# Kernel tuning notes

Measured on AMD Instinct MI355X. Metric: run time of the kernel, lower is better.

The kernel has to match this reference:

```python
import jax, jax.numpy as jnp
import numpy as np

NUM_CLASSES = 100  # matches labels fill_max
N, D = 131072, 512


def setup_inputs() -> dict:
    key = jax.random.key(0)
    kf, kl = jax.random.split(key)
    features = jax.random.normal(kf, (N, D), dtype=jnp.float32)
    labels = jax.random.randint(kl, (N,), 0, NUM_CLASSES, dtype=jnp.int64)
    return {"features": features, "labels": labels}


def reference(features, labels):
    # Per-class segment reductions: counts, sum of features, sum of squared norms.
    # trace(cov_c) = (sum_i ||x_i||^2 - n_c * ||mu_c||^2) / (n_c - 1)
    ones = jnp.ones((features.shape[0],), dtype=features.dtype)
    counts = jax.ops.segment_sum(ones, labels, num_segments=NUM_CLASSES)          # [C]
    sums = jax.ops.segment_sum(features, labels, num_segments=NUM_CLASSES)        # [C, D]
    sq = jax.ops.segment_sum(jnp.sum(features * features, axis=1), labels,
                             num_segments=NUM_CLASSES)                            # [C]
    safe_n = jnp.maximum(counts, 1.0)
    mu = sums / safe_n[:, None]                                                   # [C, D]
    ssd = sq - counts * jnp.sum(mu * mu, axis=1)                                  # sum sq deviations
    trace = ssd / jnp.maximum(counts - 1.0, 1.0)                                  # [C]
    valid = counts >= 2.0
    valid_count = jnp.sum(valid.astype(features.dtype))
    total = jnp.sum(jnp.where(valid, trace, 0.0))
    loss = jnp.where(valid_count > 0, total / jnp.maximum(valid_count, 1.0), 0.0)
    return loss
```

## Files before the change

kernel.cpp:

```cpp
#include <hip/hip_runtime.h>

#define NCLASS 100
#define DDIM   512
#define NROWS  131072

#define CHUNK   1024
#define NCHUNK  (NROWS / CHUNK)
#define NSLICE  2
#define THREADS 1024
#define NWAVES  16

__global__ __launch_bounds__(THREADS) void icv_accum_kernel(
    const float* __restrict__ feat,
    const int*   __restrict__ labels,
    float*       __restrict__ sums_p,
    float*       __restrict__ sq_p,
    int*         __restrict__ cnt_p)
{
    __shared__ int s_cnt[NCLASS];
    __shared__ int s_off[NCLASS + 1];
    __shared__ int s_pos[NCLASS];
    __shared__ int s_scan[128];
    __shared__ int s_rows[CHUNK];

    const int tid   = threadIdx.x;
    const int wave  = tid >> 6;
    const int lane  = tid & 63;
    const int slice = blockIdx.x & (NSLICE - 1);
    const int chunk = blockIdx.x >> 1;
    const int row0  = chunk * CHUNK;

    if (tid < NCLASS) s_cnt[tid] = 0;
    __syncthreads();
    const int mylab = labels[row0 + tid];
    atomicAdd(&s_cnt[mylab], 1);
    __syncthreads();

    if (tid < 128) s_scan[tid] = (tid < NCLASS) ? s_cnt[tid] : 0;
    __syncthreads();
    #pragma unroll
    for (int d = 1; d < 128; d <<= 1) {
        int v = 0;
        if (tid < 128) { v = s_scan[tid]; if (tid >= d) v += s_scan[tid - d]; }
        __syncthreads();
        if (tid < 128) s_scan[tid] = v;
        __syncthreads();
    }
    if (tid < NCLASS) {
        const int e = s_scan[tid] - s_cnt[tid];
        s_off[tid] = e;
        s_pos[tid] = e;
    }
    if (tid == NCLASS) s_off[NCLASS] = CHUNK;
    __syncthreads();
    {
        const int p = atomicAdd(&s_pos[mylab], 1);
        s_rows[p] = tid;
    }
    if (slice == 0 && tid < NCLASS)
        cnt_p[chunk * NCLASS + tid] = s_cnt[tid];
    __syncthreads();

    const int lo = wave * 6 + min(wave, 4);
    const int hi = lo + 6 + (wave < 4 ? 1 : 0);
    const int i0 = s_off[lo];
    const int i1 = s_off[hi];

    const float4* f4   = (const float4*)feat;
    const size_t  base = (size_t)row0 * (DDIM / 4) + slice * 64 + lane;

    int    c    = lo;
    int    cend = s_off[c + 1];
    float4 acc  = make_float4(0.f, 0.f, 0.f, 0.f);
    float  sq   = 0.f;

#define LOADROW(idx) f4[base + (size_t)s_rows[(idx)] * (DDIM / 4)]

#define FLUSH() do {                                                          \
        float s_ = sq;                                                        \
        s_ += __shfl_xor(s_, 32, 64); s_ += __shfl_xor(s_, 16, 64);           \
        s_ += __shfl_xor(s_,  8, 64); s_ += __shfl_xor(s_,  4, 64);           \
        s_ += __shfl_xor(s_,  2, 64); s_ += __shfl_xor(s_,  1, 64);           \
        float4* dst_ = (float4*)(sums_p                                       \
            + ((size_t)(chunk * NCLASS + c) * DDIM) + slice * 256) + lane;    \
        *dst_ = acc;                                                          \
        if (lane == 0) sq_p[(chunk * NSLICE + slice) * NCLASS + c] = s_;      \
        acc = make_float4(0.f, 0.f, 0.f, 0.f); sq = 0.f;                      \
        ++c;                                                                  \
        cend = (c <= NCLASS - 1) ? s_off[c + 1] : (CHUNK + 1);                \
    } while (0)

#define STEP(K, RING) {                                                       \
        const int i_ = ib + (K);                                              \
        if (i_ < i1) {                                                        \
            while (i_ >= cend) FLUSH();                                       \
            const float4 x_ = RING;                                           \
            const int ip_ = i_ + 4;                                           \
            if (ip_ < i1) RING = LOADROW(ip_);                                \
            acc.x += x_.x; acc.y += x_.y; acc.z += x_.z; acc.w += x_.w;       \
            sq = fmaf(x_.x, x_.x, fmaf(x_.y, x_.y,                            \
                 fmaf(x_.z, x_.z, fmaf(x_.w, x_.w, sq))));                    \
        }                                                                     \
    }

    float4 ring0 = make_float4(0.f, 0.f, 0.f, 0.f);
    float4 ring1 = ring0, ring2 = ring0, ring3 = ring0;
    if (i0 + 0 < i1) ring0 = LOADROW(i0 + 0);
    if (i0 + 1 < i1) ring1 = LOADROW(i0 + 1);
    if (i0 + 2 < i1) ring2 = LOADROW(i0 + 2);
    if (i0 + 3 < i1) ring3 = LOADROW(i0 + 3);

    for (int ib = i0; ib < i1; ib += 4) {
        STEP(0, ring0)
        STEP(1, ring1)
        STEP(2, ring2)
        STEP(3, ring3)
    }
    while (c < hi) FLUSH();
#undef STEP
#undef FLUSH
#undef LOADROW
}

__global__ __launch_bounds__(512) void icv_reduce_kernel(
    const float* __restrict__ sums_p,
    const float* __restrict__ sq_p,
    const int*   __restrict__ cnt_p,
    float*       __restrict__ cls_out)
{
    __shared__ float sred[512];
    const int c = blockIdx.x;
    const int t = threadIdx.x;

    float s = 0.f;
    const float* p = sums_p + (size_t)c * DDIM + t;
    #pragma unroll 8
    for (int ch = 0; ch < NCHUNK; ++ch)
        s += p[(size_t)ch * (NCLASS * DDIM)];
    sred[t] = s * s;
    __syncthreads();
    for (int d = 256; d > 0; d >>= 1) { if (t < d) sred[t] += sred[t + d]; __syncthreads(); }
    const float norm2 = sred[0];
    __syncthreads();

    sred[t] = (t < NCHUNK * NSLICE) ? sq_p[t * NCLASS + c] : 0.f;
    __syncthreads();
    for (int d = 256; d > 0; d >>= 1) { if (t < d) sred[t] += sred[t + d]; __syncthreads(); }
    const float sqtot = sred[0];
    __syncthreads();

    sred[t] = (t < NCHUNK) ? (float)cnt_p[t * NCLASS + c] : 0.f;
    __syncthreads();
    for (int d = 256; d > 0; d >>= 1) { if (t < d) sred[t] += sred[t + d]; __syncthreads(); }
    const float n = sred[0];

    if (t == 0) {
        const float safe  = fmaxf(n, 1.f);
        const float ssd   = sqtot - norm2 / safe;
        const float trace = ssd / fmaxf(n - 1.f, 1.f);
        const bool  valid = (n >= 2.f);
        cls_out[c * 2 + 0] = valid ? trace : 0.f;
        cls_out[c * 2 + 1] = valid ? 1.f : 0.f;
    }
}

__global__ __launch_bounds__(128) void icv_final_kernel(
    const float* __restrict__ cls_out, float* __restrict__ out)
{
    __shared__ float st[128], sv[128];
    const int t = threadIdx.x;
    st[t] = (t < NCLASS) ? cls_out[t * 2 + 0] : 0.f;
    sv[t] = (t < NCLASS) ? cls_out[t * 2 + 1] : 0.f;
    __syncthreads();
    for (int d = 64; d > 0; d >>= 1) {
        if (t < d) { st[t] += st[t + d]; sv[t] += sv[t + d]; }
        __syncthreads();
    }
    if (t == 0) out[0] = (sv[0] > 0.f) ? (st[0] / fmaxf(sv[0], 1.f)) : 0.f;
}

extern "C" void kernel_launch(void* const* d_in, const int* in_sizes, int n_in,
                              void* d_out, int out_size, void* d_ws, size_t ws_size,
                              hipStream_t stream) {
    const float* feat   = (const float*)d_in[0];
    const int*   labels = (const int*)d_in[1];
    float* out = (float*)d_out;

    float* sums_p  = (float*)d_ws;
    float* sq_p    = sums_p + (size_t)NCHUNK * NCLASS * DDIM;
    int*   cnt_p   = (int*)(sq_p + NCHUNK * NSLICE * NCLASS);
    float* cls_out = (float*)(cnt_p + NCHUNK * NCLASS);

    icv_accum_kernel<<<dim3(NCHUNK * NSLICE), THREADS, 0, stream>>>(
        feat, labels, sums_p, sq_p, cnt_p);
    icv_reduce_kernel<<<dim3(NCLASS), 512, 0, stream>>>(
        sums_p, sq_p, cnt_p, cls_out);
    icv_final_kernel<<<dim3(1), 128, 0, stream>>>(cls_out, out);
}
```

Measured before the change: 80.41 us.

## Split feature columns into four slices with 512-thread blocks and float2 loads

Work is split across four column slices instead of two, so each block of 512 threads reads float2 (8 bytes) per lane instead of float4, and each wave covers about 12 classes instead of 6. Each thread now bins two labels in the chunk, and launch bounds request 4 blocks per CU. The goal is more, smaller blocks for better occupancy and latency hiding. The cost is narrower per-lane loads, longer serial class walks per wave, duplicated label sorting across four blocks per chunk, and more sq partials for the reduce kernel, which now reads exactly 512 entries.

```diff
diff --git a/kernel.cpp b/kernel.cpp
--- a/kernel.cpp
+++ b/kernel.cpp
@@ -6,11 +6,11 @@
 
 #define CHUNK   1024
 #define NCHUNK  (NROWS / CHUNK)
-#define NSLICE  2
-#define THREADS 1024
-#define NWAVES  16
-
-__global__ __launch_bounds__(THREADS) void icv_accum_kernel(
+#define NSLICE  4
+#define THREADS 512
+#define NWAVES  8
+
+__global__ __launch_bounds__(THREADS, 4) void icv_accum_kernel(
     const float* __restrict__ feat,
     const int*   __restrict__ labels,
     float*       __restrict__ sums_p,
@@ -27,13 +27,15 @@
     const int wave  = tid >> 6;
     const int lane  = tid & 63;
     const int slice = blockIdx.x & (NSLICE - 1);
-    const int chunk = blockIdx.x >> 1;
+    const int chunk = blockIdx.x >> 2;
     const int row0  = chunk * CHUNK;
 
     if (tid < NCLASS) s_cnt[tid] = 0;
     __syncthreads();
-    const int mylab = labels[row0 + tid];
-    atomicAdd(&s_cnt[mylab], 1);
+    const int lab0 = labels[row0 + tid];
+    const int lab1 = labels[row0 + THREADS + tid];
+    atomicAdd(&s_cnt[lab0], 1);
+    atomicAdd(&s_cnt[lab1], 1);
     __syncthreads();
 
     if (tid < 128) s_scan[tid] = (tid < NCLASS) ? s_cnt[tid] : 0;
@@ -54,38 +56,40 @@
     if (tid == NCLASS) s_off[NCLASS] = CHUNK;
     __syncthreads();
     {
-        const int p = atomicAdd(&s_pos[mylab], 1);
-        s_rows[p] = tid;
+        const int p0 = atomicAdd(&s_pos[lab0], 1);
+        s_rows[p0] = tid;
+        const int p1 = atomicAdd(&s_pos[lab1], 1);
+        s_rows[p1] = THREADS + tid;
     }
     if (slice == 0 && tid < NCLASS)
         cnt_p[chunk * NCLASS + tid] = s_cnt[tid];
     __syncthreads();
 
-    const int lo = wave * 6 + min(wave, 4);
-    const int hi = lo + 6 + (wave < 4 ? 1 : 0);
+    const int lo = wave * 12 + min(wave, 4);
+    const int hi = lo + 12 + (wave < 4 ? 1 : 0);
     const int i0 = s_off[lo];
     const int i1 = s_off[hi];
 
-    const float4* f4   = (const float4*)feat;
-    const size_t  base = (size_t)row0 * (DDIM / 4) + slice * 64 + lane;
+    const float2* f2   = (const float2*)feat;
+    const size_t  base = (size_t)row0 * (DDIM / 2) + slice * 64 + lane;
 
     int    c    = lo;
     int    cend = s_off[c + 1];
-    float4 acc  = make_float4(0.f, 0.f, 0.f, 0.f);
+    float2 acc  = make_float2(0.f, 0.f);
     float  sq   = 0.f;
 
-#define LOADROW(idx) f4[base + (size_t)s_rows[(idx)] * (DDIM / 4)]
+#define LOADROW(idx) f2[base + (size_t)s_rows[(idx)] * (DDIM / 2)]
 
 #define FLUSH() do {                                                          \
         float s_ = sq;                                                        \
         s_ += __shfl_xor(s_, 32, 64); s_ += __shfl_xor(s_, 16, 64);           \
         s_ += __shfl_xor(s_,  8, 64); s_ += __shfl_xor(s_,  4, 64);           \
         s_ += __shfl_xor(s_,  2, 64); s_ += __shfl_xor(s_,  1, 64);           \
-        float4* dst_ = (float4*)(sums_p                                       \
-            + ((size_t)(chunk * NCLASS + c) * DDIM) + slice * 256) + lane;    \
+        float2* dst_ = (float2*)(sums_p                                       \
+            + ((size_t)(chunk * NCLASS + c) * DDIM) + slice * 128) + lane;    \
         *dst_ = acc;                                                          \
         if (lane == 0) sq_p[(chunk * NSLICE + slice) * NCLASS + c] = s_;      \
-        acc = make_float4(0.f, 0.f, 0.f, 0.f); sq = 0.f;                      \
+        acc = make_float2(0.f, 0.f); sq = 0.f;                                \
         ++c;                                                                  \
         cend = (c <= NCLASS - 1) ? s_off[c + 1] : (CHUNK + 1);                \
     } while (0)
@@ -94,17 +98,16 @@
         const int i_ = ib + (K);                                              \
         if (i_ < i1) {                                                        \
             while (i_ >= cend) FLUSH();                                       \
-            const float4 x_ = RING;                                           \
+            const float2 x_ = RING;                                           \
             const int ip_ = i_ + 4;                                           \
             if (ip_ < i1) RING = LOADROW(ip_);                                \
-            acc.x += x_.x; acc.y += x_.y; acc.z += x_.z; acc.w += x_.w;       \
-            sq = fmaf(x_.x, x_.x, fmaf(x_.y, x_.y,                            \
-                 fmaf(x_.z, x_.z, fmaf(x_.w, x_.w, sq))));                    \
+            acc.x += x_.x; acc.y += x_.y;                                     \
+            sq = fmaf(x_.x, x_.x, fmaf(x_.y, x_.y, sq));                      \
         }                                                                     \
     }
 
-    float4 ring0 = make_float4(0.f, 0.f, 0.f, 0.f);
-    float4 ring1 = ring0, ring2 = ring0, ring3 = ring0;
+    float2 ring0 = make_float2(0.f, 0.f);
+    float2 ring1 = ring0, ring2 = ring0, ring3 = ring0;
     if (i0 + 0 < i1) ring0 = LOADROW(i0 + 0);
     if (i0 + 1 < i1) ring1 = LOADROW(i0 + 1);
     if (i0 + 2 < i1) ring2 = LOADROW(i0 + 2);
@@ -143,7 +146,7 @@
     const float norm2 = sred[0];
     __syncthreads();
 
-    sred[t] = (t < NCHUNK * NSLICE) ? sq_p[t * NCLASS + c] : 0.f;
+    sred[t] = sq_p[t * NCLASS + c];
     __syncthreads();
     for (int d = 256; d > 0; d >>= 1) { if (t < d) sred[t] += sred[t + d]; __syncthreads(); }
     const float sqtot = sred[0];
```

Result: slower. 105.4 us (+31.1%).

## Split label sort into separate kernel, balance waves by rows, deepen prefetch, fuse final reduce

Applied to the files above, without the earlier changes.

Moves the per-chunk counting sort of labels into its own kernel that writes sorted row indices, class offsets and per-wave class spans to workspace. The accumulation kernel then assigns classes to waves by row position instead of a fixed class split, which evens out the work per wave. It also widens the prefetch ring from 4 to 8 rows. The reduce kernel uses wave shuffles instead of shared-memory tree reductions, and the final kernel is folded in through a last-block atomic counter. The costs are an extra kernel launch plus workspace traffic for the sort results, and more registers for the deeper ring.

```diff
diff --git a/kernel.cpp b/kernel.cpp
--- a/kernel.cpp
+++ b/kernel.cpp
@@ -4,18 +4,20 @@
 #define DDIM   512
 #define NROWS  131072
 
-#define CHUNK   1024
-#define NCHUNK  (NROWS / CHUNK)
-#define NSLICE  2
-#define THREADS 1024
-#define NWAVES  16
-
-__global__ __launch_bounds__(THREADS) void icv_accum_kernel(
-    const float* __restrict__ feat,
-    const int*   __restrict__ labels,
-    float*       __restrict__ sums_p,
-    float*       __restrict__ sq_p,
-    int*         __restrict__ cnt_p)
+#define CHUNK    1024
+#define NCHUNK   (NROWS / CHUNK)
+#define NSLICE   2
+#define ATHREADS 1024
+#define NWAVES   16
+#define SPAN     (CHUNK / NWAVES)
+
+__global__ __launch_bounds__(CHUNK) void icv_sort_kernel(
+    const int* __restrict__ labels,
+    int* __restrict__ rows_g,
+    int* __restrict__ off_g,
+    int* __restrict__ cnt_p,
+    int* __restrict__ span_g,
+    int* __restrict__ sync_cnt)
 {
     __shared__ int s_cnt[NCLASS];
     __shared__ int s_off[NCLASS + 1];
@@ -24,16 +26,15 @@
     __shared__ int s_rows[CHUNK];
 
     const int tid   = threadIdx.x;
-    const int wave  = tid >> 6;
-    const int lane  = tid & 63;
-    const int slice = blockIdx.x & (NSLICE - 1);
-    const int chunk = blockIdx.x >> 1;
+    const int chunk = blockIdx.x;
     const int row0  = chunk * CHUNK;
 
     if (tid < NCLASS) s_cnt[tid] = 0;
-    __syncthreads();
-    const int mylab = labels[row0 + tid];
-    atomicAdd(&s_cnt[mylab], 1);
+    if (chunk == 0 && tid == 0) *sync_cnt = 0;
+    __syncthreads();
+
+    const int lab = labels[row0 + tid];
+    atomicAdd(&s_cnt[lab], 1);
     __syncthreads();
 
     if (tid < 128) s_scan[tid] = (tid < NCLASS) ? s_cnt[tid] : 0;
@@ -46,35 +47,68 @@
         if (tid < 128) s_scan[tid] = v;
         __syncthreads();
     }
+    if (tid < NCLASS) { const int e = s_scan[tid] - s_cnt[tid]; s_off[tid] = e; s_pos[tid] = e; }
+    if (tid == NCLASS) s_off[NCLASS] = CHUNK;
+    __syncthreads();
+
+    { const int p = atomicAdd(&s_pos[lab], 1); s_rows[p] = row0 + tid; }
+
+    if (tid < NWAVES) {
+        int cf = NCLASS, ce = NCLASS;
+        for (int c = 0; c < NCLASS; ++c) {
+            int ow = s_off[c] / SPAN; if (ow > NWAVES - 1) ow = NWAVES - 1;
+            if (ow == tid && cf == NCLASS) cf = c;
+            if (ow > tid) { ce = c; break; }
+        }
+        if (cf > ce) cf = ce;
+        span_g[(chunk * NWAVES + tid) * 2 + 0] = cf;
+        span_g[(chunk * NWAVES + tid) * 2 + 1] = ce;
+    }
+    __syncthreads();
+
+    rows_g[chunk * CHUNK + tid] = s_rows[tid];
     if (tid < NCLASS) {
-        const int e = s_scan[tid] - s_cnt[tid];
-        s_off[tid] = e;
-        s_pos[tid] = e;
-    }
-    if (tid == NCLASS) s_off[NCLASS] = CHUNK;
-    __syncthreads();
-    {
-        const int p = atomicAdd(&s_pos[mylab], 1);
-        s_rows[p] = tid;
-    }
-    if (slice == 0 && tid < NCLASS)
-        cnt_p[chunk * NCLASS + tid] = s_cnt[tid];
-    __syncthreads();
-
-    const int lo = wave * 6 + min(wave, 4);
-    const int hi = lo + 6 + (wave < 4 ? 1 : 0);
-    const int i0 = s_off[lo];
-    const int i1 = s_off[hi];
-
-    const float4* f4   = (const float4*)feat;
-    const size_t  base = (size_t)row0 * (DDIM / 4) + slice * 64 + lane;
-
-    int    c    = lo;
-    int    cend = s_off[c + 1];
+        off_g[chunk * (NCLASS + 1) + tid] = s_off[tid];
+        cnt_p[chunk * NCLASS + tid]       = s_cnt[tid];
+    }
+    if (tid == NCLASS) off_g[chunk * (NCLASS + 1) + NCLASS] = CHUNK;
+}
+
+__global__ __launch_bounds__(ATHREADS) void icv_accum_kernel(
+    const float* __restrict__ feat,
+    const int*   __restrict__ rows_g,
+    const int*   __restrict__ off_g,
+    const int*   __restrict__ span_g,
+    float*       __restrict__ sums_p,
+    float*       __restrict__ sq_p)
+{
+    __shared__ int s_rows[CHUNK];
+    __shared__ int s_off[NCLASS + 1];
+
+    const int tid   = threadIdx.x;
+    const int wave  = tid >> 6;
+    const int lane  = tid & 63;
+    const int slice = blockIdx.x & (NSLICE - 1);
+    const int chunk = blockIdx.x >> 1;
+
+    s_rows[tid] = rows_g[chunk * CHUNK + tid];
+    if (tid < NCLASS + 1) s_off[tid] = off_g[chunk * (NCLASS + 1) + tid];
+    __syncthreads();
+
+    const int cf = span_g[(chunk * NWAVES + wave) * 2 + 0];
+    const int ce = span_g[(chunk * NWAVES + wave) * 2 + 1];
+    const int i0 = s_off[cf];
+    const int i1 = s_off[ce];
+
+    const float4* f4      = (const float4*)feat;
+    const int     colbase = slice * 64 + lane;
+
+    int    c    = cf;
+    int    cend = (c < ce) ? s_off[c + 1] : (CHUNK + 1);
     float4 acc  = make_float4(0.f, 0.f, 0.f, 0.f);
     float  sq   = 0.f;
 
-#define LOADROW(idx) f4[base + (size_t)s_rows[(idx)] * (DDIM / 4)]
+#define LOADROW(idx) f4[(size_t)s_rows[(idx)] * (DDIM / 4) + colbase]
 
 #define FLUSH() do {                                                          \
         float s_ = sq;                                                        \
@@ -87,7 +121,7 @@
         if (lane == 0) sq_p[(chunk * NSLICE + slice) * NCLASS + c] = s_;      \
         acc = make_float4(0.f, 0.f, 0.f, 0.f); sq = 0.f;                      \
         ++c;                                                                  \
-        cend = (c <= NCLASS - 1) ? s_off[c + 1] : (CHUNK + 1);                \
+        cend = (c < ce) ? s_off[c + 1] : (CHUNK + 1);                         \
     } while (0)
 
 #define STEP(K, RING) {                                                       \
@@ -95,7 +129,7 @@
         if (i_ < i1) {                                                        \
             while (i_ >= cend) FLUSH();                                       \
             const float4 x_ = RING;                                           \
-            const int ip_ = i_ + 4;                                           \
+            const int ip_ = i_ + 8;                                           \
             if (ip_ < i1) RING = LOADROW(ip_);                                \
             acc.x += x_.x; acc.y += x_.y; acc.z += x_.z; acc.w += x_.w;       \
             sq = fmaf(x_.x, x_.x, fmaf(x_.y, x_.y,                            \
@@ -103,20 +137,22 @@
         }                                                                     \
     }
 
-    float4 ring0 = make_float4(0.f, 0.f, 0.f, 0.f);
-    float4 ring1 = ring0, ring2 = ring0, ring3 = ring0;
-    if (i0 + 0 < i1) ring0 = LOADROW(i0 + 0);
-    if (i0 + 1 < i1) ring1 = LOADROW(i0 + 1);
-    if (i0 + 2 < i1) ring2 = LOADROW(i0 + 2);
-    if (i0 + 3 < i1) ring3 = LOADROW(i0 + 3);
-
-    for (int ib = i0; ib < i1; ib += 4) {
-        STEP(0, ring0)
-        STEP(1, ring1)
-        STEP(2, ring2)
-        STEP(3, ring3)
-    }
-    while (c < hi) FLUSH();
+    float4 r0 = make_float4(0.f, 0.f, 0.f, 0.f);
+    float4 r1 = r0, r2 = r0, r3 = r0, r4 = r0, r5 = r0, r6 = r0, r7 = r0;
+    if (i0 + 0 < i1) r0 = LOADROW(i0 + 0);
+    if (i0 + 1 < i1) r1 = LOADROW(i0 + 1);
+    if (i0 + 2 < i1) r2 = LOADROW(i0 + 2);
+    if (i0 + 3 < i1) r3 = LOADROW(i0 + 3);
+    if (i0 + 4 < i1) r4 = LOADROW(i0 + 4);
+    if (i0 + 5 < i1) r5 = LOADROW(i0 + 5);
+    if (i0 + 6 < i1) r6 = LOADROW(i0 + 6);
+    if (i0 + 7 < i1) r7 = LOADROW(i0 + 7);
+
+    for (int ib = i0; ib < i1; ib += 8) {
+        STEP(0, r0) STEP(1, r1) STEP(2, r2) STEP(3, r3)
+        STEP(4, r4) STEP(5, r5) STEP(6, r6) STEP(7, r7)
+    }
+    while (c < ce) FLUSH();
 #undef STEP
 #undef FLUSH
 #undef LOADROW
@@ -126,57 +162,75 @@
     const float* __restrict__ sums_p,
     const float* __restrict__ sq_p,
     const int*   __restrict__ cnt_p,
-    float*       __restrict__ cls_out)
+    float*       __restrict__ cls_out,
+    int*         __restrict__ sync_cnt,
+    float*       __restrict__ out)
 {
-    __shared__ float sred[512];
-    const int c = blockIdx.x;
-    const int t = threadIdx.x;
+    __shared__ float red[3][8];
+    __shared__ float fin[2][8];
+    __shared__ int   s_last;
+
+    const int c    = blockIdx.x;
+    const int t    = threadIdx.x;
+    const int wave = t >> 6;
+    const int lane = t & 63;
 
     float s = 0.f;
     const float* p = sums_p + (size_t)c * DDIM + t;
     #pragma unroll 8
     for (int ch = 0; ch < NCHUNK; ++ch)
         s += p[(size_t)ch * (NCLASS * DDIM)];
-    sred[t] = s * s;
-    __syncthreads();
-    for (int d = 256; d > 0; d >>= 1) { if (t < d) sred[t] += sred[t + d]; __syncthreads(); }
-    const float norm2 = sred[0];
-    __syncthreads();
-
-    sred[t] = (t < NCHUNK * NSLICE) ? sq_p[t * NCLASS + c] : 0.f;
-    __syncthreads();
-    for (int d = 256; d > 0; d >>= 1) { if (t < d) sred[t] += sred[t + d]; __syncthreads(); }
-    const float sqtot = sred[0];
-    __syncthreads();
-
-    sred[t] = (t < NCHUNK) ? (float)cnt_p[t * NCLASS + c] : 0.f;
-    __syncthreads();
-    for (int d = 256; d > 0; d >>= 1) { if (t < d) sred[t] += sred[t + d]; __syncthreads(); }
-    const float n = sred[0];
+
+    float v1 = s * s;
+    float v2 = (t < NCHUNK * NSLICE) ? sq_p[t * NCLASS + c] : 0.f;
+    float v3 = (t < NCHUNK) ? (float)cnt_p[t * NCLASS + c] : 0.f;
+    #pragma unroll
+    for (int off = 32; off > 0; off >>= 1) {
+        v1 += __shfl_xor(v1, off, 64);
+        v2 += __shfl_xor(v2, off, 64);
+        v3 += __shfl_xor(v3, off, 64);
+    }
+    if (lane == 0) { red[0][wave] = v1; red[1][wave] = v2; red[2][wave] = v3; }
+    __syncthreads();
 
     if (t == 0) {
+        float n2 = 0.f, sq = 0.f, n = 0.f;
+        #pragma unroll
+        for (int w = 0; w < 8; ++w) { n2 += red[0][w]; sq += red[1][w]; n += red[2][w]; }
         const float safe  = fmaxf(n, 1.f);
-        const float ssd   = sqtot - norm2 / safe;
+        const float ssd   = sq - n2 / safe;
         const float trace = ssd / fmaxf(n - 1.f, 1.f);
         const bool  valid = (n >= 2.f);
         cls_out[c * 2 + 0] = valid ? trace : 0.f;
         cls_out[c * 2 + 1] = valid ? 1.f : 0.f;
-    }
-}
-
-__global__ __launch_bounds__(128) void icv_final_kernel(
-    const float* __restrict__ cls_out, float* __restrict__ out)
-{
-    __shared__ float st[128], sv[128];
-    const int t = threadIdx.x;
-    st[t] = (t < NCLASS) ? cls_out[t * 2 + 0] : 0.f;
-    sv[t] = (t < NCLASS) ? cls_out[t * 2 + 1] : 0.f;
-    __syncthreads();
-    for (int d = 64; d > 0; d >>= 1) {
-        if (t < d) { st[t] += st[t + d]; sv[t] += sv[t + d]; }
+        __threadfence();
+        const int done = atomicAdd(sync_cnt, 1);
+        s_last = (done == NCLASS - 1) ? 1 : 0;
+    }
+    __syncthreads();
+
+    if (s_last) {
+        __threadfence();
+        float tv = 0.f, vv = 0.f;
+        if (t < NCLASS) {
+            const volatile float* cv = (const volatile float*)cls_out;
+            tv = cv[t * 2 + 0];
+            vv = cv[t * 2 + 1];
+        }
+        #pragma unroll
+        for (int off = 32; off > 0; off >>= 1) {
+            tv += __shfl_xor(tv, off, 64);
+            vv += __shfl_xor(vv, off, 64);
+        }
+        if (lane == 0) { fin[0][wave] = tv; fin[1][wave] = vv; }
         __syncthreads();
-    }
-    if (t == 0) out[0] = (sv[0] > 0.f) ? (st[0] / fmaxf(sv[0], 1.f)) : 0.f;
+        if (t == 0) {
+            float tot = 0.f, vc = 0.f;
+            #pragma unroll
+            for (int w = 0; w < 8; ++w) { tot += fin[0][w]; vc += fin[1][w]; }
+            out[0] = (vc > 0.f) ? (tot / fmaxf(vc, 1.f)) : 0.f;
+        }
+    }
 }
 
 extern "C" void kernel_launch(void* const* d_in, const int* in_sizes, int n_in,
@@ -189,11 +243,16 @@
     float* sums_p  = (float*)d_ws;
     float* sq_p    = sums_p + (size_t)NCHUNK * NCLASS * DDIM;
     int*   cnt_p   = (int*)(sq_p + NCHUNK * NSLICE * NCLASS);
-    float* cls_out = (float*)(cnt_p + NCHUNK * NCLASS);
-
-    icv_accum_kernel<<<dim3(NCHUNK * NSLICE), THREADS, 0, stream>>>(
-        feat, labels, sums_p, sq_p, cnt_p);
+    int*   rows_g  = cnt_p + NCHUNK * NCLASS;
+    int*   off_g   = rows_g + NCHUNK * CHUNK;
+    int*   span_g  = off_g + NCHUNK * (NCLASS + 1);
+    float* cls_out = (float*)(span_g + NCHUNK * NWAVES * 2);
+    int*   sync_cnt= (int*)(cls_out + NCLASS * 2);
+
+    icv_sort_kernel<<<dim3(NCHUNK), CHUNK, 0, stream>>>(
+        labels, rows_g, off_g, cnt_p, span_g, sync_cnt);
+    icv_accum_kernel<<<dim3(NCHUNK * NSLICE), ATHREADS, 0, stream>>>(
+        feat, rows_g, off_g, span_g, sums_p, sq_p);
     icv_reduce_kernel<<<dim3(NCLASS), 512, 0, stream>>>(
-        sums_p, sq_p, cnt_p, cls_out);
-    icv_final_kernel<<<dim3(1), 128, 0, stream>>>(cls_out, out);
-}
+        sums_p, sq_p, cnt_p, cls_out, sync_cnt, out);
+}
```

Result: slower. 84.77 us (+5.4%).
